# Kernel tuning notes

Measured on AMD Instinct MI355X. Metric: run time of the kernel, lower is better.

The kernel has to match this reference:

```python
import jax, jax.numpy as jnp
import numpy as np

BS, NCAM, N, S = 2, 3, 64, 256


def setup_inputs() -> dict:
    key = jax.random.key(0)
    ks = jax.random.split(key, 7)
    # 2D projected points in pixel coordinates [0, image_size)
    points = jax.random.uniform(ks[0], (BS, NCAM, N, 2), dtype=jnp.float32) * S
    # blob params (per-point), realistic trained-model ranges
    sigmas = jax.random.uniform(ks[1], (BS, N), dtype=jnp.float32) * 0.05 + 0.02
    exponents = jax.random.uniform(ks[2], (BS, N), dtype=jnp.float32) * 0.5 + 0.75
    intensities = jax.random.uniform(ks[3], (BS, N), dtype=jnp.float32) * 0.5 + 0.5
    # per-camera scale factors, near 1
    camera_sigmas = jax.random.uniform(ks[4], (BS, NCAM), dtype=jnp.float32) * 0.2 + 0.9
    camera_exponents = jax.random.uniform(ks[5], (BS, NCAM), dtype=jnp.float32) * 0.2 + 0.9
    camera_intensities = jax.random.uniform(ks[6], (BS, NCAM), dtype=jnp.float32) * 0.2 + 0.9
    return {
        "points": points,
        "sigmas": sigmas,
        "exponents": exponents,
        "intensities": intensities,
        "camera_sigmas": camera_sigmas,
        "camera_exponents": camera_exponents,
        "camera_intensities": camera_intensities,
        "image_size": S,
    }


def reference(points, sigmas, exponents, intensities,
              camera_sigmas, camera_exponents, camera_intensities, image_size):
    """Faithful JAX port of render_points (render_mode='gaussians')."""
    bs, ncam, n = points.shape[0], points.shape[1], points.shape[2]
    s2 = image_size // 2
    # normalize pixel coords to [-1, 1] and flatten batch*cameras
    p = jnp.clip((points - s2) / s2, -1.0, 1.0).reshape(bs * ncam, n, 2)
    # per-point params scaled by per-camera factors; repeat_interleave(3,0)
    # on (bs,N) == broadcast over camera axis then flatten -> (bs*3, N, 1, 1)
    sig = (sigmas[:, None, :] * camera_sigmas[:, :, None]).reshape(bs * ncam, n, 1, 1)
    expn = (exponents[:, None, :] * camera_exponents[:, :, None]).reshape(bs * ncam, n, 1, 1)
    inten = (intensities[:, None, :] * camera_intensities[:, :, None]).reshape(bs * ncam, n, 1, 1)
    grid = jnp.linspace(-1.0, 1.0, image_size, dtype=jnp.float32)
    # m[y, x] = (grid[x], grid[y]); squared distance to each point
    dx = grid[None, None, None, :] - p[:, :, 0, None, None]   # (bs*3, N, 1, W)
    dy = grid[None, None, :, None] - p[:, :, 1, None, None]   # (bs*3, N, H, 1)
    dst = dx * dx + dy * dy                                   # (bs*3, N, H, W)
    blobs = jnp.exp(-((dst / (2.0 * sig * sig)) ** expn))      # (bs*3, N, H, W)
    masks = jnp.minimum(jnp.max(blobs * inten, axis=1), 1.0)   # amax over N, clamp(max=1)
    masks = masks.reshape(bs, ncam, image_size, image_size)
    blobs = blobs.reshape(bs, ncam, n, image_size, image_size)
    return masks, blobs
```

## Files before the change

kernel.cpp:

```cpp
#include <hip/hip_runtime.h>

constexpr int S_IMG = 256;
constexpr int NPT   = 64;
constexpr int BC    = 6;
constexpr int NCAM_ = 3;

typedef float vf2 __attribute__((ext_vector_type(2)));
typedef float vf4 __attribute__((ext_vector_type(4)));

__device__ __forceinline__ float blob_eval(float u, float e) {
    float v = exp2f(e * __log2f(u));
    return exp2f(-1.4426950408889634f * v);
}

__global__ __launch_bounds__(128) void render_fused(
    const float* __restrict__ points,
    const float* __restrict__ sigmas,
    const float* __restrict__ exponents,
    const float* __restrict__ intensities,
    const float* __restrict__ cam_sig,
    const float* __restrict__ cam_exp,
    const float* __restrict__ cam_int,
    float* __restrict__ masks,
    float* __restrict__ blobs)
{
    const int blk = blockIdx.x;
    const int bc  = blk >> 8;
    const int y   = blk & 255;
    const int b   = bc / NCAM_;
    const int t   = threadIdx.x;

    __shared__ vf4 sP[NPT];
    __shared__ vf2 sQ[NPT];
    if (t < NPT) {
        float px = points[(bc * NPT + t) * 2 + 0];
        float py = points[(bc * NPT + t) * 2 + 1];
        px = fminf(fmaxf((px - 128.0f) * (1.0f / 128.0f), -1.0f), 1.0f);
        py = fminf(fmaxf((py - 128.0f) * (1.0f / 128.0f), -1.0f), 1.0f);
        float sg = sigmas[b * NPT + t] * cam_sig[bc];
        float e  = exponents[b * NPT + t] * cam_exp[bc];
        vf4 P;
        P.x = px;
        P.y = py;
        P.z = 1.0f / (2.0f * sg * sg);
        P.w = exp2f(3.2034f / e);
        sP[t] = P;
        vf2 Q;
        Q.x = e;
        Q.y = intensities[b * NPT + t] * cam_int[bc];
        sQ[t] = Q;
    }
    __syncthreads();

    const int x = t << 1;

    const float step = 2.0f / 255.0f;
    const float gx0  = fmaf((float)x, step, -1.0f);
    const float gx1  = gx0 + step;
    const float gy   = fmaf((float)y, step, -1.0f);

    float m0 = 0.0f, m1 = 0.0f;
    float* bp = blobs + ((size_t)bc * NPT << 16) + ((size_t)y << 8) + x;
    const size_t nstride = (size_t)S_IMG * S_IMG;

    #pragma unroll 4
    for (int n = 0; n < NPT; ++n) {
        vf4 P = sP[n];
        float dx0  = gx0 - P.x;
        float dx1  = gx1 - P.x;
        float dyv  = gy  - P.y;
        float kdy2 = P.z * dyv * dyv;
        float u0   = fmaf(P.z * dx0, dx0, kdy2);
        float u1   = fmaf(P.z * dx1, dx1, kdy2);
        vf2 o; o.x = 0.0f; o.y = 0.0f;
        if (fminf(u0, u1) < P.w) {
            vf2 Q = sQ[n];
            o.x = blob_eval(u0, Q.x);
            o.y = blob_eval(u1, Q.x);
            m0 = fmaxf(m0, o.x * Q.y);
            m1 = fmaxf(m1, o.y * Q.y);
        }
        __builtin_nontemporal_store(o, reinterpret_cast<vf2*>(bp + n * nstride));
    }

    vf2 mm;
    mm.x = fminf(m0, 1.0f);
    mm.y = fminf(m1, 1.0f);
    *reinterpret_cast<vf2*>(masks + ((size_t)bc << 16)
                                  + ((size_t)y << 8) + x) = mm;
}

extern "C" void kernel_launch(void* const* d_in, const int* in_sizes, int n_in,
                              void* d_out, int out_size, void* d_ws, size_t ws_size,
                              hipStream_t stream) {
    const float* points      = (const float*)d_in[0];
    const float* sigmas      = (const float*)d_in[1];
    const float* exponents   = (const float*)d_in[2];
    const float* intensities = (const float*)d_in[3];
    const float* cam_sig     = (const float*)d_in[4];
    const float* cam_exp     = (const float*)d_in[5];
    const float* cam_int     = (const float*)d_in[6];

    float* masks = (float*)d_out;
    float* blobs = (float*)d_out + (size_t)BC * S_IMG * S_IMG;

    dim3 grid(BC * S_IMG);
    dim3 block(128);
    render_fused<<<grid, block, 0, stream>>>(
        points, sigmas, exponents, intensities, cam_sig, cam_exp, cam_int,
        masks, blobs);
}
```

Baseline: 24.85 us.

## Split points across thread halves with 4-wide stores and shared-memory mask reduction

Each block now covers two image rows with 256 threads. Each thread handles four pixels, and the two halves of the block each process 32 of the 64 points. The per-half maxima are combined through shared memory before the mask is written. Blob stores widen to 16-byte vectors and are no longer marked nontemporal. The goal is wider memory transactions and less per-point setup per pixel, at the cost of an extra barrier and a possible change in cache behaviour for the streaming writes.

```diff
diff --git a/kernel.cpp b/kernel.cpp
--- a/kernel.cpp
+++ b/kernel.cpp
@@ -13,7 +13,7 @@
     return exp2f(-1.4426950408889634f * v);
 }
 
-__global__ __launch_bounds__(128) void render_fused(
+__global__ __launch_bounds__(256) void render_fused(
     const float* __restrict__ points,
     const float* __restrict__ sigmas,
     const float* __restrict__ exponents,
@@ -25,13 +25,14 @@
     float* __restrict__ blobs)
 {
     const int blk = blockIdx.x;
-    const int bc  = blk >> 8;
-    const int y   = blk & 255;
+    const int bc  = blk >> 7;
+    const int y0  = (blk & 127) << 1;
     const int b   = bc / NCAM_;
     const int t   = threadIdx.x;
 
     __shared__ vf4 sP[NPT];
     __shared__ vf2 sQ[NPT];
+    __shared__ vf4 sM[128];
     if (t < NPT) {
         float px = points[(bc * NPT + t) * 2 + 0];
         float py = points[(bc * NPT + t) * 2 + 1];
@@ -52,42 +53,66 @@
     }
     __syncthreads();
 
-    const int x = t << 1;
+    const int half  = t >> 7;
+    const int tt    = t & 127;
+    const int nbase = half << 5;
+    const int lin   = tt << 2;
+    const int y     = y0 + (lin >> 8);
+    const int x     = lin & 255;
 
     const float step = 2.0f / 255.0f;
-    const float gx0  = fmaf((float)x, step, -1.0f);
-    const float gx1  = gx0 + step;
     const float gy   = fmaf((float)y, step, -1.0f);
+    float gx[4];
+    #pragma unroll
+    for (int j = 0; j < 4; ++j) gx[j] = fmaf((float)(x + j), step, -1.0f);
 
-    float m0 = 0.0f, m1 = 0.0f;
-    float* bp = blobs + ((size_t)bc * NPT << 16) + ((size_t)y << 8) + x;
+    float m0 = 0.0f, m1 = 0.0f, m2 = 0.0f, m3 = 0.0f;
+    float* bp = blobs + ((size_t)(bc * NPT + nbase) << 16)
+                      + ((size_t)y << 8) + x;
     const size_t nstride = (size_t)S_IMG * S_IMG;
 
     #pragma unroll 4
-    for (int n = 0; n < NPT; ++n) {
-        vf4 P = sP[n];
-        float dx0  = gx0 - P.x;
-        float dx1  = gx1 - P.x;
-        float dyv  = gy  - P.y;
+    for (int i = 0; i < 32; ++i) {
+        vf4 P = sP[nbase + i];
+        float dyv  = gy - P.y;
         float kdy2 = P.z * dyv * dyv;
-        float u0   = fmaf(P.z * dx0, dx0, kdy2);
-        float u1   = fmaf(P.z * dx1, dx1, kdy2);
-        vf2 o; o.x = 0.0f; o.y = 0.0f;
-        if (fminf(u0, u1) < P.w) {
-            vf2 Q = sQ[n];
+        float dx0 = gx[0] - P.x, dx1 = gx[1] - P.x;
+        float dx2 = gx[2] - P.x, dx3 = gx[3] - P.x;
+        float u0 = fmaf(P.z * dx0, dx0, kdy2);
+        float u1 = fmaf(P.z * dx1, dx1, kdy2);
+        float u2 = fmaf(P.z * dx2, dx2, kdy2);
+        float u3 = fmaf(P.z * dx3, dx3, kdy2);
+        vf4 o; o.x = 0.0f; o.y = 0.0f; o.z = 0.0f; o.w = 0.0f;
+        float umin = fminf(fminf(u0, u1), fminf(u2, u3));
+        if (umin < P.w) {
+            vf2 Q = sQ[nbase + i];
             o.x = blob_eval(u0, Q.x);
             o.y = blob_eval(u1, Q.x);
+            o.z = blob_eval(u2, Q.x);
+            o.w = blob_eval(u3, Q.x);
             m0 = fmaxf(m0, o.x * Q.y);
             m1 = fmaxf(m1, o.y * Q.y);
+            m2 = fmaxf(m2, o.z * Q.y);
+            m3 = fmaxf(m3, o.w * Q.y);
         }
-        __builtin_nontemporal_store(o, reinterpret_cast<vf2*>(bp + n * nstride));
+        *reinterpret_cast<vf4*>(bp + i * nstride) = o;
     }
 
-    vf2 mm;
-    mm.x = fminf(m0, 1.0f);
-    mm.y = fminf(m1, 1.0f);
-    *reinterpret_cast<vf2*>(masks + ((size_t)bc << 16)
-                                  + ((size_t)y << 8) + x) = mm;
+    if (half == 0) {
+        vf4 mv; mv.x = m0; mv.y = m1; mv.z = m2; mv.w = m3;
+        sM[tt] = mv;
+    }
+    __syncthreads();
+    if (half == 1) {
+        vf4 p = sM[tt];
+        vf4 mm;
+        mm.x = fminf(fmaxf(m0, p.x), 1.0f);
+        mm.y = fminf(fmaxf(m1, p.y), 1.0f);
+        mm.z = fminf(fmaxf(m2, p.z), 1.0f);
+        mm.w = fminf(fmaxf(m3, p.w), 1.0f);
+        *reinterpret_cast<vf4*>(masks + ((size_t)bc << 16)
+                                      + ((size_t)y << 8) + x) = mm;
+    }
 }
 
 extern "C" void kernel_launch(void* const* d_in, const int* in_sizes, int n_in,
@@ -104,8 +129,8 @@
     float* masks = (float*)d_out;
     float* blobs = (float*)d_out + (size_t)BC * S_IMG * S_IMG;
 
-    dim3 grid(BC * S_IMG);
-    dim3 block(128);
+    dim3 grid(BC * (S_IMG / 2));
+    dim3 block(256);
     render_fused<<<grid, block, 0, stream>>>(
         points, sigmas, exponents, intensities, cam_sig, cam_exp, cam_int,
         masks, blobs);
```

New measurement: 21.38 us. 14.0% less time.

## Split blob slices and mask rows into separate interleaved block roles

Applied to the files above, without the earlier changes.

Interleaves two block types in one grid. Even blocks each write half of one point's 256x256 blob slice as contiguous float4 rows. Odd blocks compute two mask rows by re-evaluating all 64 blobs per pixel. This replaces the old per-row blocks, which wrote 64 strided slices each, with contiguous writes and drops the nontemporal hint. The cost is that every blob value is computed twice, once for the blob output and once for the mask reduction.

```diff
diff --git a/kernel.cpp b/kernel.cpp
--- a/kernel.cpp
+++ b/kernel.cpp
@@ -13,7 +13,7 @@
     return exp2f(-1.4426950408889634f * v);
 }
 
-__global__ __launch_bounds__(128) void render_fused(
+__global__ __launch_bounds__(256) void render_split(
     const float* __restrict__ points,
     const float* __restrict__ sigmas,
     const float* __restrict__ exponents,
@@ -24,70 +24,121 @@
     float* __restrict__ masks,
     float* __restrict__ blobs)
 {
-    const int blk = blockIdx.x;
-    const int bc  = blk >> 8;
-    const int y   = blk & 255;
-    const int b   = bc / NCAM_;
-    const int t   = threadIdx.x;
+    const int blk  = blockIdx.x;
+    const int t    = threadIdx.x;
+    const float step = 2.0f / 255.0f;
 
-    __shared__ vf4 sP[NPT];
-    __shared__ vf2 sQ[NPT];
-    if (t < NPT) {
-        float px = points[(bc * NPT + t) * 2 + 0];
-        float py = points[(bc * NPT + t) * 2 + 1];
+    if ((blk & 1) == 0) {
+        const int sl    = blk >> 1;
+        const int slice = sl >> 1;
+        const int half  = sl & 1;
+        const int bc    = slice >> 6;
+        const int n     = slice & 63;
+        const int b     = bc / NCAM_;
+
+        float px = points[slice * 2 + 0];
+        float py = points[slice * 2 + 1];
         px = fminf(fmaxf((px - 128.0f) * (1.0f / 128.0f), -1.0f), 1.0f);
         py = fminf(fmaxf((py - 128.0f) * (1.0f / 128.0f), -1.0f), 1.0f);
-        float sg = sigmas[b * NPT + t] * cam_sig[bc];
-        float e  = exponents[b * NPT + t] * cam_exp[bc];
-        vf4 P;
-        P.x = px;
-        P.y = py;
-        P.z = 1.0f / (2.0f * sg * sg);
-        P.w = exp2f(3.2034f / e);
-        sP[t] = P;
-        vf2 Q;
-        Q.x = e;
-        Q.y = intensities[b * NPT + t] * cam_int[bc];
-        sQ[t] = Q;
+        float sg = sigmas[b * NPT + n] * cam_sig[bc];
+        float k  = 1.0f / (2.0f * sg * sg);
+        float e  = exponents[b * NPT + n] * cam_exp[bc];
+        float rn = exp2f(3.2034f / e);
+
+        const int w     = t >> 6;
+        const int lane  = t & 63;
+        const int x0    = lane << 2;
+        const int ybase = (half << 7) + (w << 5);
+
+        float kdx2[4];
+        #pragma unroll
+        for (int j = 0; j < 4; ++j) {
+            float gx = fmaf((float)(x0 + j), step, -1.0f);
+            float dx = gx - px;
+            kdx2[j] = k * dx * dx;
+        }
+
+        float* bp = blobs + ((size_t)slice << 16) + ((size_t)ybase << 8) + x0;
+
+        #pragma unroll 4
+        for (int i = 0; i < 32; ++i) {
+            float gy   = fmaf((float)(ybase + i), step, -1.0f);
+            float dyv  = gy - py;
+            float kdy2 = k * dyv * dyv;
+            float u0 = kdx2[0] + kdy2;
+            float u1 = kdx2[1] + kdy2;
+            float u2 = kdx2[2] + kdy2;
+            float u3 = kdx2[3] + kdy2;
+            vf4 o; o.x = 0.0f; o.y = 0.0f; o.z = 0.0f; o.w = 0.0f;
+            if (fminf(fminf(u0, u1), fminf(u2, u3)) < rn) {
+                o.x = blob_eval(u0, e);
+                o.y = blob_eval(u1, e);
+                o.z = blob_eval(u2, e);
+                o.w = blob_eval(u3, e);
+            }
+            *reinterpret_cast<vf4*>(bp + (i << 8)) = o;
+        }
+    } else {
+        const int mask_idx = blk >> 1;
+        const int bc = mask_idx >> 7;
+        const int y0 = (mask_idx & 127) << 1;
+        const int b  = bc / NCAM_;
+
+        __shared__ vf4 sP[NPT];
+        __shared__ vf2 sQ[NPT];
+        if (t < NPT) {
+            float px = points[(bc * NPT + t) * 2 + 0];
+            float py = points[(bc * NPT + t) * 2 + 1];
+            px = fminf(fmaxf((px - 128.0f) * (1.0f / 128.0f), -1.0f), 1.0f);
+            py = fminf(fmaxf((py - 128.0f) * (1.0f / 128.0f), -1.0f), 1.0f);
+            float sg = sigmas[b * NPT + t] * cam_sig[bc];
+            float e  = exponents[b * NPT + t] * cam_exp[bc];
+            vf4 P;
+            P.x = px;
+            P.y = py;
+            P.z = 1.0f / (2.0f * sg * sg);
+            P.w = exp2f(3.2034f / e);
+            sP[t] = P;
+            vf2 Q;
+            Q.x = e;
+            Q.y = intensities[b * NPT + t] * cam_int[bc];
+            sQ[t] = Q;
+        }
+        __syncthreads();
+
+        const int lin = t << 1;
+        const int y   = y0 + (lin >> 8);
+        const int x   = lin & 255;
+
+        const float gx0 = fmaf((float)x, step, -1.0f);
+        const float gx1 = gx0 + step;
+        const float gy  = fmaf((float)y, step, -1.0f);
+
+        float m0 = 0.0f, m1 = 0.0f;
+        #pragma unroll 4
+        for (int n = 0; n < NPT; ++n) {
+            vf4 P = sP[n];
+            float dx0  = gx0 - P.x;
+            float dx1  = gx1 - P.x;
+            float dyv  = gy  - P.y;
+            float kdy2 = P.z * dyv * dyv;
+            float u0   = fmaf(P.z * dx0, dx0, kdy2);
+            float u1   = fmaf(P.z * dx1, dx1, kdy2);
+            if (fminf(u0, u1) < P.w) {
+                vf2 Q = sQ[n];
+                float b0 = blob_eval(u0, Q.x);
+                float b1 = blob_eval(u1, Q.x);
+                m0 = fmaxf(m0, b0 * Q.y);
+                m1 = fmaxf(m1, b1 * Q.y);
+            }
+        }
+
+        vf2 mm;
+        mm.x = fminf(m0, 1.0f);
+        mm.y = fminf(m1, 1.0f);
+        *reinterpret_cast<vf2*>(masks + ((size_t)bc << 16)
+                                      + ((size_t)y << 8) + x) = mm;
     }
-    __syncthreads();
-
-    const int x = t << 1;
-
-    const float step = 2.0f / 255.0f;
-    const float gx0  = fmaf((float)x, step, -1.0f);
-    const float gx1  = gx0 + step;
-    const float gy   = fmaf((float)y, step, -1.0f);
-
-    float m0 = 0.0f, m1 = 0.0f;
-    float* bp = blobs + ((size_t)bc * NPT << 16) + ((size_t)y << 8) + x;
-    const size_t nstride = (size_t)S_IMG * S_IMG;
-
-    #pragma unroll 4
-    for (int n = 0; n < NPT; ++n) {
-        vf4 P = sP[n];
-        float dx0  = gx0 - P.x;
-        float dx1  = gx1 - P.x;
-        float dyv  = gy  - P.y;
-        float kdy2 = P.z * dyv * dyv;
-        float u0   = fmaf(P.z * dx0, dx0, kdy2);
-        float u1   = fmaf(P.z * dx1, dx1, kdy2);
-        vf2 o; o.x = 0.0f; o.y = 0.0f;
-        if (fminf(u0, u1) < P.w) {
-            vf2 Q = sQ[n];
-            o.x = blob_eval(u0, Q.x);
-            o.y = blob_eval(u1, Q.x);
-            m0 = fmaxf(m0, o.x * Q.y);
-            m1 = fmaxf(m1, o.y * Q.y);
-        }
-        __builtin_nontemporal_store(o, reinterpret_cast<vf2*>(bp + n * nstride));
-    }
-
-    vf2 mm;
-    mm.x = fminf(m0, 1.0f);
-    mm.y = fminf(m1, 1.0f);
-    *reinterpret_cast<vf2*>(masks + ((size_t)bc << 16)
-                                  + ((size_t)y << 8) + x) = mm;
 }
 
 extern "C" void kernel_launch(void* const* d_in, const int* in_sizes, int n_in,
@@ -104,9 +155,9 @@
     float* masks = (float*)d_out;
     float* blobs = (float*)d_out + (size_t)BC * S_IMG * S_IMG;
 
-    dim3 grid(BC * S_IMG);
-    dim3 block(128);
-    render_fused<<<grid, block, 0, stream>>>(
+    dim3 grid(1536);
+    dim3 block(256);
+    render_split<<<grid, block, 0, stream>>>(
         points, sigmas, exponents, intensities, cam_sig, cam_exp, cam_int,
         masks, blobs);
 }
```

Measured after the change: 31.76 us. 27.8% more time.
